# Optimization experiments

Measured on AMD Instinct MI355X. Metric: run time of the kernel, lower is better.

The kernel has to match this reference:

```python
import jax, jax.numpy as jnp
import numpy as np

NUM_CAPSULE = 16
DIM_CAPSULE = 64
ROUTINGS = 3
T_EPS = 1e-07


def squash(v, axis=-1):
    # NOTE: this repo's 'squash' is v / sqrt(||v||^2 + eps) (norm-only scaling)
    s = jnp.sum(v * v, axis=axis, keepdims=True)
    return v / jnp.sqrt(s + T_EPS)


def setup_inputs() -> dict:
    key = jax.random.key(0)
    k1, k2 = jax.random.split(key)
    B, N_in, D_in = 64, 512, 1024
    x = jax.random.normal(k1, (B, N_in, D_in), dtype=jnp.float32)
    # xavier-normal-ish init for W [1, D_in, num_capsule*dim_capsule]
    fan_in, fan_out = D_in, NUM_CAPSULE * DIM_CAPSULE
    std = float(np.sqrt(2.0 / (fan_in + fan_out)))
    W = jax.random.normal(k2, (1, D_in, NUM_CAPSULE * DIM_CAPSULE), dtype=jnp.float32) * std
    return {"x": x, "W": W}


def reference(x, W):
    B, N_in, D_in = x.shape
    # u_hat: [B, N_in, num_cap*dim_cap] -> [B, num_cap, N_in, dim_cap]
    u_hat = jnp.matmul(x, W[0])
    u_hat = u_hat.reshape(B, N_in, NUM_CAPSULE, DIM_CAPSULE).transpose(0, 2, 1, 3)
    b = jnp.zeros((B, NUM_CAPSULE, N_in), dtype=u_hat.dtype)
    outputs = None
    for i in range(ROUTINGS):
        # torch code permutes to [B, N_in, num_cap], softmaxes dim=2, permutes back:
        # equivalent to softmax over the num_capsule axis (axis=1)
        c = jax.nn.softmax(b, axis=1)  # [B, num_cap, N_in]
        outputs = squash(jnp.einsum('bij,bijk->bik', c, u_hat))  # [B, num_cap, dim_cap]
        if i < ROUTINGS - 1:
            b = jnp.einsum('bik,bijk->bij', outputs, u_hat)  # [B, num_cap, N_in]
    return outputs
```

## Files before the change

kernel.cpp:

```cpp
#include <hip/hip_runtime.h>
#include <stdint.h>

#define NUM_CAP 16
#define DIM_CAP 64
#define BATCH   64
#define N_IN    512
#define D_IN    1024
#define N_COL   1024
#define M_ROWS  (BATCH*N_IN)

typedef __attribute__((ext_vector_type(8))) short short8;
typedef __attribute__((ext_vector_type(4))) float f32x4;

__device__ __forceinline__ float bf2f(unsigned int u) {
  return __uint_as_float(u << 16);
}
__device__ __forceinline__ unsigned short f2bf_rne(float f) {
  unsigned int x = __float_as_uint(f);
  x += 0x7fffu + ((x >> 16) & 1u);
  return (unsigned short)(x >> 16);
}
__device__ __forceinline__ unsigned int pack_trunc(unsigned int lo, unsigned int hi) {
  return (lo >> 16) | (hi & 0xffff0000u);
}

__global__ void transpose_w(const float* __restrict__ W,
                            unsigned short* __restrict__ Wt) {
  __shared__ float tile[32][33];
  const int tx = threadIdx.x, ty = threadIdx.y;
  const int bx = blockIdx.x, by = blockIdx.y;
  tile[ty][tx] = W[(by * 32 + ty) * N_COL + bx * 32 + tx];
  __syncthreads();
  Wt[(bx * 32 + ty) * D_IN + by * 32 + tx] = f2bf_rne(tile[tx][ty]);
}

__global__ __launch_bounds__(256) void gemm_uhat(
    const float* __restrict__ A,
    const unsigned short* __restrict__ Bt,
    unsigned short* __restrict__ C) {
  __shared__ __align__(16) unsigned short lA[128 * 32];
  __shared__ __align__(16) unsigned short lB[128 * 32];

  const int t = threadIdx.x;
  const int wave = t >> 6, lane = t & 63;
  const int xcd = blockIdx.x & 7, local = blockIdx.x >> 3;
  const int mt = xcd * 32 + (local >> 3), nt = local & 7;
  const int m0 = mt * 128, n0 = nt * 128;
  const int wm = wave & 1, wn = wave >> 1;

  f32x4 acc[4][4] = {};

  const int ar = t >> 1, ah = t & 1;
  const float* agp = A + (size_t)(m0 + ar) * D_IN + ah * 16;
  const int xrA = (ar >> 1) & 3;
  unsigned short* lap0 = lA + ar * 32 + ((2 * ah + 0) ^ xrA) * 8;
  unsigned short* lap1 = lA + ar * 32 + ((2 * ah + 1) ^ xrA) * 8;

  const int srow = lane >> 2;
  const int schunk = ((lane & 3) ^ ((srow >> 1) & 3)) * 8;

  for (int kt = 0; kt < D_IN / 32; ++kt) {
    const int k0 = kt * 32;
    __syncthreads();
    const uint4 a0 = *(const uint4*)(agp + k0);
    const uint4 a1 = *(const uint4*)(agp + k0 + 4);
    const uint4 a2 = *(const uint4*)(agp + k0 + 8);
    const uint4 a3 = *(const uint4*)(agp + k0 + 12);
    uint4 p0, p1;
    p0.x = pack_trunc(a0.x, a0.y); p0.y = pack_trunc(a0.z, a0.w);
    p0.z = pack_trunc(a1.x, a1.y); p0.w = pack_trunc(a1.z, a1.w);
    p1.x = pack_trunc(a2.x, a2.y); p1.y = pack_trunc(a2.z, a2.w);
    p1.z = pack_trunc(a3.x, a3.y); p1.w = pack_trunc(a3.z, a3.w);
    *(uint4*)lap0 = p0;
    *(uint4*)lap1 = p1;
    #pragma unroll
    for (int s0 = 0; s0 < 2; ++s0) {
      const int s = wave + s0 * 4;
      const unsigned short* gb = Bt + (size_t)(n0 + s * 16 + srow) * D_IN + k0 + schunk;
      __builtin_amdgcn_global_load_lds(
          (const __attribute__((address_space(1))) void*)gb,
          (__attribute__((address_space(3))) void*)(lB + s * 512), 16, 0, 0);
    }
    __syncthreads();

    short8 af[4], bfr[4];
    const int rsel = lane & 15;
    const int q = lane >> 4;
    const int koff = (q ^ ((rsel >> 1) & 3)) * 8;
    #pragma unroll
    for (int tm = 0; tm < 4; tm++)
      af[tm] = *(const short8*)&lA[(wm * 64 + tm * 16 + rsel) * 32 + koff];
    #pragma unroll
    for (int tn = 0; tn < 4; tn++)
      bfr[tn] = *(const short8*)&lB[(wn * 64 + tn * 16 + rsel) * 32 + koff];
    #pragma unroll
    for (int tm = 0; tm < 4; tm++)
      #pragma unroll
      for (int tn = 0; tn < 4; tn++)
        acc[tm][tn] = __builtin_amdgcn_mfma_f32_16x16x32_bf16(
            af[tm], bfr[tn], acc[tm][tn], 0, 0, 0);
  }

  const int lrow = (lane >> 4) * 4, lcol = lane & 15;
  #pragma unroll
  for (int tm = 0; tm < 4; tm++)
    #pragma unroll
    for (int tn = 0; tn < 4; tn++)
      #pragma unroll
      for (int r = 0; r < 4; r++) {
        const int row = m0 + wm * 64 + tm * 16 + lrow + r;
        const int col = n0 + wn * 64 + tn * 16 + lcol;
        C[(size_t)row * N_COL + col] = f2bf_rne(acc[tm][tn][r]);
      }
}

__global__ __launch_bounds__(256) void route_partial(
    const unsigned short* __restrict__ uhat,
    const float* __restrict__ prev,
    float* __restrict__ P,
    const int first) {
  __shared__ float red[4][1024];
  const int t = threadIdx.x;
  const int w = t >> 6, lane = t & 63;
  const int b = blockIdx.x >> 4, jt4 = blockIdx.x & 15;
  const int jt = jt4 * 4 + w;
  const int i_l = lane >> 2, c4 = lane & 3;

  float pv[16];
  if (!first) {
    const float* pp = prev + (b * NUM_CAP + i_l) * DIM_CAP + c4 * 16;
    #pragma unroll
    for (int q = 0; q < 16; q++) pv[q] = pp[q];
  }
  float acc[16];
  #pragma unroll
  for (int q = 0; q < 16; q++) acc[q] = 0.f;

  const unsigned short* ub =
      uhat + (size_t)(b * N_IN + jt * 8) * N_COL + lane * 16;

  for (int jj = 0; jj < 8; ++jj, ub += N_COL) {
    const uint4 d0 = *(const uint4*)ub;
    const uint4 d1 = *(const uint4*)(ub + 8);
    float u[16];
    #define UNP(wd, o) { u[(o)] = bf2f((wd) & 0xffffu); u[(o)+1] = __uint_as_float((wd) & 0xffff0000u); }
    UNP(d0.x, 0) UNP(d0.y, 2) UNP(d0.z, 4) UNP(d0.w, 6)
    UNP(d1.x, 8) UNP(d1.y, 10) UNP(d1.z, 12) UNP(d1.w, 14)
    #undef UNP

    float c;
    if (first) {
      c = 0.0625f;
    } else {
      float dot = 0.f;
      #pragma unroll
      for (int q = 0; q < 16; q++) dot = fmaf(pv[q], u[q], dot);
      dot += __shfl_xor(dot, 1);
      dot += __shfl_xor(dot, 2);
      float m = dot;
      #pragma unroll
      for (int d = 4; d < 64; d <<= 1) m = fmaxf(m, __shfl_xor(m, d));
      const float e = __expf(dot - m);
      float s = e;
      #pragma unroll
      for (int d = 4; d < 64; d <<= 1) s += __shfl_xor(s, d);
      c = e / s;
    }
    #pragma unroll
    for (int q = 0; q < 16; q++) acc[q] = fmaf(c, u[q], acc[q]);
  }

  #pragma unroll
  for (int q = 0; q < 4; q++)
    *(float4*)&red[w][lane * 16 + q * 4] = make_float4(
        acc[q * 4 + 0], acc[q * 4 + 1], acc[q * 4 + 2], acc[q * 4 + 3]);
  __syncthreads();
  const float4 r0 = *(const float4*)&red[0][t * 4];
  const float4 r1 = *(const float4*)&red[1][t * 4];
  const float4 r2 = *(const float4*)&red[2][t * 4];
  const float4 r3 = *(const float4*)&red[3][t * 4];
  float4 s;
  s.x = r0.x + r1.x + r2.x + r3.x;
  s.y = r0.y + r1.y + r2.y + r3.y;
  s.z = r0.z + r1.z + r2.z + r3.z;
  s.w = r0.w + r1.w + r2.w + r3.w;
  *(float4*)&P[(size_t)blockIdx.x * 1024 + t * 4] = s;
}

__global__ __launch_bounds__(64) void route_reduce(
    const float* __restrict__ P, float* __restrict__ dst) {
  const int bi = blockIdx.x;
  const int k = threadIdx.x;
  const int b = bi >> 4, i = bi & 15;
  const float* p = P + (size_t)b * 16 * 1024 + i * 64 + k;
  float s = 0.f;
  #pragma unroll
  for (int tt = 0; tt < 16; ++tt) s += p[(size_t)tt * 1024];
  float ss = s * s;
  #pragma unroll
  for (int d = 1; d < 64; d <<= 1) ss += __shfl_xor(ss, d);
  dst[bi * 64 + k] = s / sqrtf(ss + 1e-7f);
}

extern "C" void kernel_launch(void* const* d_in, const int* in_sizes, int n_in,
                              void* d_out, int out_size, void* d_ws, size_t ws_size,
                              hipStream_t stream) {
  const float* x = (const float*)d_in[0];
  const float* W = (const float*)d_in[1];
  float* out = (float*)d_out;

  char* ws = (char*)d_ws;
  unsigned short* Wt   = (unsigned short*)ws;
  unsigned short* uhat = (unsigned short*)(ws + (size_t)(2 << 20));
  float* P    = (float*)(ws + (size_t)66 * (1 << 20));
  float* prev = (float*)(ws + (size_t)70 * (1 << 20));

  transpose_w<<<dim3(32, 32), dim3(32, 32), 0, stream>>>(W, Wt);
  gemm_uhat<<<2048, 256, 0, stream>>>(x, Wt, uhat);

  route_partial<<<1024, 256, 0, stream>>>(uhat, prev, P, 1);
  route_reduce<<<1024, 64, 0, stream>>>(P, prev);
  route_partial<<<1024, 256, 0, stream>>>(uhat, prev, P, 0);
  route_reduce<<<1024, 64, 0, stream>>>(P, prev);
  route_partial<<<1024, 256, 0, stream>>>(uhat, prev, P, 0);
  route_reduce<<<1024, 64, 0, stream>>>(P, out);
}
```

Measured before the change: 374.2 us.

## Fuse routing iterations into one per-batch kernel and prefetch A tiles in GEMM

```diff
diff --git a/kernel.cpp b/kernel.cpp
--- a/kernel.cpp
+++ b/kernel.cpp
@@ -59,13 +59,14 @@
   const int srow = lane >> 2;
   const int schunk = ((lane & 3) ^ ((srow >> 1) & 3)) * 8;
 
+  uint4 a0 = *(const uint4*)(agp);
+  uint4 a1 = *(const uint4*)(agp + 4);
+  uint4 a2 = *(const uint4*)(agp + 8);
+  uint4 a3 = *(const uint4*)(agp + 12);
+
   for (int kt = 0; kt < D_IN / 32; ++kt) {
     const int k0 = kt * 32;
     __syncthreads();
-    const uint4 a0 = *(const uint4*)(agp + k0);
-    const uint4 a1 = *(const uint4*)(agp + k0 + 4);
-    const uint4 a2 = *(const uint4*)(agp + k0 + 8);
-    const uint4 a3 = *(const uint4*)(agp + k0 + 12);
     uint4 p0, p1;
     p0.x = pack_trunc(a0.x, a0.y); p0.y = pack_trunc(a0.z, a0.w);
     p0.z = pack_trunc(a1.x, a1.y); p0.w = pack_trunc(a1.z, a1.w);
@@ -83,6 +84,12 @@
     }
     __syncthreads();
 
+    const int kn = ((kt + 1) & 31) * 32;
+    a0 = *(const uint4*)(agp + kn);
+    a1 = *(const uint4*)(agp + kn + 4);
+    a2 = *(const uint4*)(agp + kn + 8);
+    a3 = *(const uint4*)(agp + kn + 12);
+
     short8 af[4], bfr[4];
     const int rsel = lane & 15;
     const int q = lane >> 4;
@@ -114,92 +121,86 @@
       }
 }
 
-__global__ __launch_bounds__(256) void route_partial(
+__global__ __launch_bounds__(1024) void route_all(
     const unsigned short* __restrict__ uhat,
-    const float* __restrict__ prev,
-    float* __restrict__ P,
-    const int first) {
-  __shared__ float red[4][1024];
+    float* __restrict__ out) {
+  __shared__ float red[16][1028];
+  __shared__ float sq[16][68];
   const int t = threadIdx.x;
   const int w = t >> 6, lane = t & 63;
-  const int b = blockIdx.x >> 4, jt4 = blockIdx.x & 15;
-  const int jt = jt4 * 4 + w;
+  const int b = blockIdx.x;
   const int i_l = lane >> 2, c4 = lane & 3;
-
-  float pv[16];
-  if (!first) {
-    const float* pp = prev + (b * NUM_CAP + i_l) * DIM_CAP + c4 * 16;
-    #pragma unroll
-    for (int q = 0; q < 16; q++) pv[q] = pp[q];
+  const int oi = t >> 6, ok = t & 63;
+
+  const unsigned short* ub0 =
+      uhat + (size_t)(b * N_IN + w * 32) * N_COL + lane * 16;
+
+  for (int it = 0; it < 3; ++it) {
+    float pv[16];
+    if (it) {
+      #pragma unroll
+      for (int q = 0; q < 4; q++)
+        *(float4*)&pv[q * 4] = *(const float4*)&sq[i_l][c4 * 16 + q * 4];
+    }
+    float acc[16];
+    #pragma unroll
+    for (int q = 0; q < 16; q++) acc[q] = 0.f;
+
+    const unsigned short* ub = ub0;
+    for (int jj = 0; jj < 32; ++jj, ub += N_COL) {
+      const uint4 d0 = *(const uint4*)ub;
+      const uint4 d1 = *(const uint4*)(ub + 8);
+      float u[16];
+      #define UNP(wd, o) { u[(o)] = bf2f((wd) & 0xffffu); u[(o)+1] = __uint_as_float((wd) & 0xffff0000u); }
+      UNP(d0.x, 0) UNP(d0.y, 2) UNP(d0.z, 4) UNP(d0.w, 6)
+      UNP(d1.x, 8) UNP(d1.y, 10) UNP(d1.z, 12) UNP(d1.w, 14)
+      #undef UNP
+
+      float c;
+      if (it == 0) {
+        c = 0.0625f;
+      } else {
+        float dot = 0.f;
+        #pragma unroll
+        for (int q = 0; q < 16; q++) dot = fmaf(pv[q], u[q], dot);
+        dot += __shfl_xor(dot, 1);
+        dot += __shfl_xor(dot, 2);
+        float m = dot;
+        #pragma unroll
+        for (int d = 4; d < 64; d <<= 1) m = fmaxf(m, __shfl_xor(m, d));
+        const float e = __expf(dot - m);
+        float s = e;
+        #pragma unroll
+        for (int d = 4; d < 64; d <<= 1) s += __shfl_xor(s, d);
+        c = e / s;
+      }
+      #pragma unroll
+      for (int q = 0; q < 16; q++) acc[q] = fmaf(c, u[q], acc[q]);
+    }
+
+    #pragma unroll
+    for (int q = 0; q < 4; q++)
+      *(float4*)&red[w][i_l * 64 + c4 * 16 + q * 4] = make_float4(
+          acc[q * 4 + 0], acc[q * 4 + 1], acc[q * 4 + 2], acc[q * 4 + 3]);
+    __syncthreads();
+
+    float s = 0.f;
+    #pragma unroll
+    for (int ww = 0; ww < 16; ++ww) s += red[ww][t];
+
+    float ss = s * s;
+    #pragma unroll
+    for (int d = 1; d < 64; d <<= 1) ss += __shfl_xor(ss, d);
+    const float v = s / sqrtf(ss + 1e-7f);
+
+    __syncthreads();
+    if (it < 2) {
+      sq[oi][ok] = v;
+      __syncthreads();
+    } else {
+      out[b * 1024 + t] = v;
+    }
   }
-  float acc[16];
-  #pragma unroll
-  for (int q = 0; q < 16; q++) acc[q] = 0.f;
-
-  const unsigned short* ub =
-      uhat + (size_t)(b * N_IN + jt * 8) * N_COL + lane * 16;
-
-  for (int jj = 0; jj < 8; ++jj, ub += N_COL) {
-    const uint4 d0 = *(const uint4*)ub;
-    const uint4 d1 = *(const uint4*)(ub + 8);
-    float u[16];
-    #define UNP(wd, o) { u[(o)] = bf2f((wd) & 0xffffu); u[(o)+1] = __uint_as_float((wd) & 0xffff0000u); }
-    UNP(d0.x, 0) UNP(d0.y, 2) UNP(d0.z, 4) UNP(d0.w, 6)
-    UNP(d1.x, 8) UNP(d1.y, 10) UNP(d1.z, 12) UNP(d1.w, 14)
-    #undef UNP
-
-    float c;
-    if (first) {
-      c = 0.0625f;
-    } else {
-      float dot = 0.f;
-      #pragma unroll
-      for (int q = 0; q < 16; q++) dot = fmaf(pv[q], u[q], dot);
-      dot += __shfl_xor(dot, 1);
-      dot += __shfl_xor(dot, 2);
-      float m = dot;
-      #pragma unroll
-      for (int d = 4; d < 64; d <<= 1) m = fmaxf(m, __shfl_xor(m, d));
-      const float e = __expf(dot - m);
-      float s = e;
-      #pragma unroll
-      for (int d = 4; d < 64; d <<= 1) s += __shfl_xor(s, d);
-      c = e / s;
-    }
-    #pragma unroll
-    for (int q = 0; q < 16; q++) acc[q] = fmaf(c, u[q], acc[q]);
-  }
-
-  #pragma unroll
-  for (int q = 0; q < 4; q++)
-    *(float4*)&red[w][lane * 16 + q * 4] = make_float4(
-        acc[q * 4 + 0], acc[q * 4 + 1], acc[q * 4 + 2], acc[q * 4 + 3]);
-  __syncthreads();
-  const float4 r0 = *(const float4*)&red[0][t * 4];
-  const float4 r1 = *(const float4*)&red[1][t * 4];
-  const float4 r2 = *(const float4*)&red[2][t * 4];
-  const float4 r3 = *(const float4*)&red[3][t * 4];
-  float4 s;
-  s.x = r0.x + r1.x + r2.x + r3.x;
-  s.y = r0.y + r1.y + r2.y + r3.y;
-  s.z = r0.z + r1.z + r2.z + r3.z;
-  s.w = r0.w + r1.w + r2.w + r3.w;
-  *(float4*)&P[(size_t)blockIdx.x * 1024 + t * 4] = s;
-}
-
-__global__ __launch_bounds__(64) void route_reduce(
-    const float* __restrict__ P, float* __restrict__ dst) {
-  const int bi = blockIdx.x;
-  const int k = threadIdx.x;
-  const int b = bi >> 4, i = bi & 15;
-  const float* p = P + (size_t)b * 16 * 1024 + i * 64 + k;
-  float s = 0.f;
-  #pragma unroll
-  for (int tt = 0; tt < 16; ++tt) s += p[(size_t)tt * 1024];
-  float ss = s * s;
-  #pragma unroll
-  for (int d = 1; d < 64; d <<= 1) ss += __shfl_xor(ss, d);
-  dst[bi * 64 + k] = s / sqrtf(ss + 1e-7f);
 }
 
 extern "C" void kernel_launch(void* const* d_in, const int* in_sizes, int n_in,
@@ -212,16 +213,8 @@
   char* ws = (char*)d_ws;
   unsigned short* Wt   = (unsigned short*)ws;
   unsigned short* uhat = (unsigned short*)(ws + (size_t)(2 << 20));
-  float* P    = (float*)(ws + (size_t)66 * (1 << 20));
-  float* prev = (float*)(ws + (size_t)70 * (1 << 20));
 
   transpose_w<<<dim3(32, 32), dim3(32, 32), 0, stream>>>(W, Wt);
   gemm_uhat<<<2048, 256, 0, stream>>>(x, Wt, uhat);
-
-  route_partial<<<1024, 256, 0, stream>>>(uhat, prev, P, 1);
-  route_reduce<<<1024, 64, 0, stream>>>(P, prev);
-  route_partial<<<1024, 256, 0, stream>>>(uhat, prev, P, 0);
-  route_reduce<<<1024, 64, 0, stream>>>(P, prev);
-  route_partial<<<1024, 256, 0, stream>>>(uhat, prev, P, 0);
-  route_reduce<<<1024, 64, 0, stream>>>(P, out);
-}
+  route_all<<<BATCH, 1024, 0, stream>>>(uhat, out);
+}
```

Result: no change. 371.9 us (-0.6%).

## Pre-convert x to bf16, fuse first routing pass into GEMM epilogue

Applied to the files above, without the earlier changes.

```diff
diff --git a/kernel.cpp b/kernel.cpp
--- a/kernel.cpp
+++ b/kernel.cpp
@@ -20,8 +20,21 @@
   x += 0x7fffu + ((x >> 16) & 1u);
   return (unsigned short)(x >> 16);
 }
-__device__ __forceinline__ unsigned int pack_trunc(unsigned int lo, unsigned int hi) {
-  return (lo >> 16) | (hi & 0xffff0000u);
+__device__ __forceinline__ unsigned int pack_rne(unsigned int lo, unsigned int hi) {
+  const unsigned int lr = lo + (0x7fffu + ((lo >> 16) & 1u));
+  const unsigned int hr = hi + (0x7fffu + ((hi >> 16) & 1u));
+  return (lr >> 16) | (hr & 0xffff0000u);
+}
+
+__global__ __launch_bounds__(256) void conv_x(const float* __restrict__ x,
+                                              unsigned short* __restrict__ xb) {
+  const size_t i = ((size_t)blockIdx.x * 256 + threadIdx.x) * 8;
+  const uint4 a = *(const uint4*)(x + i);
+  const uint4 b = *(const uint4*)(x + i + 4);
+  uint4 p;
+  p.x = pack_rne(a.x, a.y); p.y = pack_rne(a.z, a.w);
+  p.z = pack_rne(b.x, b.y); p.w = pack_rne(b.z, b.w);
+  *(uint4*)(xb + i) = p;
 }
 
 __global__ void transpose_w(const float* __restrict__ W,
@@ -34,12 +47,19 @@
   Wt[(bx * 32 + ty) * D_IN + by * 32 + tx] = f2bf_rne(tile[tx][ty]);
 }
 
+__global__ __launch_bounds__(256) void zero_s1(float* __restrict__ S1) {
+  *(float4*)(S1 + ((size_t)blockIdx.x * 256 + threadIdx.x) * 4) =
+      make_float4(0.f, 0.f, 0.f, 0.f);
+}
+
 __global__ __launch_bounds__(256) void gemm_uhat(
-    const float* __restrict__ A,
+    const unsigned short* __restrict__ A,
     const unsigned short* __restrict__ Bt,
-    unsigned short* __restrict__ C) {
+    unsigned short* __restrict__ C,
+    float* __restrict__ S1) {
   __shared__ __align__(16) unsigned short lA[128 * 32];
   __shared__ __align__(16) unsigned short lB[128 * 32];
+  __shared__ float cs[128];
 
   const int t = threadIdx.x;
   const int wave = t >> 6, lane = t & 63;
@@ -48,13 +68,9 @@
   const int m0 = mt * 128, n0 = nt * 128;
   const int wm = wave & 1, wn = wave >> 1;
 
+  if (t < 128) cs[t] = 0.f;
+
   f32x4 acc[4][4] = {};
-
-  const int ar = t >> 1, ah = t & 1;
-  const float* agp = A + (size_t)(m0 + ar) * D_IN + ah * 16;
-  const int xrA = (ar >> 1) & 3;
-  unsigned short* lap0 = lA + ar * 32 + ((2 * ah + 0) ^ xrA) * 8;
-  unsigned short* lap1 = lA + ar * 32 + ((2 * ah + 1) ^ xrA) * 8;
 
   const int srow = lane >> 2;
   const int schunk = ((lane & 3) ^ ((srow >> 1) & 3)) * 8;
@@ -62,20 +78,13 @@
   for (int kt = 0; kt < D_IN / 32; ++kt) {
     const int k0 = kt * 32;
     __syncthreads();
-    const uint4 a0 = *(const uint4*)(agp + k0);
-    const uint4 a1 = *(const uint4*)(agp + k0 + 4);
-    const uint4 a2 = *(const uint4*)(agp + k0 + 8);
-    const uint4 a3 = *(const uint4*)(agp + k0 + 12);
-    uint4 p0, p1;
-    p0.x = pack_trunc(a0.x, a0.y); p0.y = pack_trunc(a0.z, a0.w);
-    p0.z = pack_trunc(a1.x, a1.y); p0.w = pack_trunc(a1.z, a1.w);
-    p1.x = pack_trunc(a2.x, a2.y); p1.y = pack_trunc(a2.z, a2.w);
-    p1.z = pack_trunc(a3.x, a3.y); p1.w = pack_trunc(a3.z, a3.w);
-    *(uint4*)lap0 = p0;
-    *(uint4*)lap1 = p1;
     #pragma unroll
     for (int s0 = 0; s0 < 2; ++s0) {
       const int s = wave + s0 * 4;
+      const unsigned short* ga = A + (size_t)(m0 + s * 16 + srow) * D_IN + k0 + schunk;
+      __builtin_amdgcn_global_load_lds(
+          (const __attribute__((address_space(1))) void*)ga,
+          (__attribute__((address_space(3))) void*)(lA + s * 512), 16, 0, 0);
       const unsigned short* gb = Bt + (size_t)(n0 + s * 16 + srow) * D_IN + k0 + schunk;
       __builtin_amdgcn_global_load_lds(
           (const __attribute__((address_space(1))) void*)gb,
@@ -112,13 +121,27 @@
         const int col = n0 + wn * 64 + tn * 16 + lcol;
         C[(size_t)row * N_COL + col] = f2bf_rne(acc[tm][tn][r]);
       }
-}
-
-__global__ __launch_bounds__(256) void route_partial(
+
+  #pragma unroll
+  for (int tn = 0; tn < 4; tn++) {
+    float p = 0.f;
+    #pragma unroll
+    for (int tm = 0; tm < 4; tm++)
+      #pragma unroll
+      for (int r = 0; r < 4; r++) p += acc[tm][tn][r];
+    atomicAdd(&cs[wn * 64 + tn * 16 + lcol], p);
+  }
+  __syncthreads();
+  if (t < 128)
+    atomicAdd(&S1[(size_t)(mt >> 2) * N_COL + n0 + t], cs[t] * 0.0625f);
+}
+
+__global__ __launch_bounds__(256) void route_mid(
     const unsigned short* __restrict__ uhat,
-    const float* __restrict__ prev,
-    float* __restrict__ P,
-    const int first) {
+    const float* __restrict__ Vin,
+    float* __restrict__ Pout,
+    const int mode) {
+  __shared__ float sq[16 * 68];
   __shared__ float red[4][1024];
   const int t = threadIdx.x;
   const int w = t >> 6, lane = t & 63;
@@ -126,12 +149,30 @@
   const int jt = jt4 * 4 + w;
   const int i_l = lane >> 2, c4 = lane & 3;
 
+  float4 v4;
+  if (mode == 0) {
+    v4 = *(const float4*)&Vin[(size_t)b * 1024 + t * 4];
+  } else {
+    v4 = make_float4(0.f, 0.f, 0.f, 0.f);
+    #pragma unroll
+    for (int s = 0; s < 16; ++s) {
+      const float4 ps = *(const float4*)&Vin[((size_t)b * 16 + s) * 1024 + t * 4];
+      v4.x += ps.x; v4.y += ps.y; v4.z += ps.z; v4.w += ps.w;
+    }
+  }
+  float ss = v4.x * v4.x + v4.y * v4.y + v4.z * v4.z + v4.w * v4.w;
+  #pragma unroll
+  for (int d = 1; d < 16; d <<= 1) ss += __shfl_xor(ss, d);
+  const float inv = 1.f / sqrtf(ss + 1e-7f);
+  const int oi = t >> 4, ok = (t & 15) * 4;
+  *(float4*)&sq[oi * 68 + ok] = make_float4(v4.x * inv, v4.y * inv, v4.z * inv, v4.w * inv);
+  __syncthreads();
+
   float pv[16];
-  if (!first) {
-    const float* pp = prev + (b * NUM_CAP + i_l) * DIM_CAP + c4 * 16;
-    #pragma unroll
-    for (int q = 0; q < 16; q++) pv[q] = pp[q];
-  }
+  #pragma unroll
+  for (int q = 0; q < 4; q++)
+    *(float4*)&pv[q * 4] = *(const float4*)&sq[i_l * 68 + c4 * 16 + q * 4];
+
   float acc[16];
   #pragma unroll
   for (int q = 0; q < 16; q++) acc[q] = 0.f;
@@ -148,24 +189,16 @@
     UNP(d1.x, 8) UNP(d1.y, 10) UNP(d1.z, 12) UNP(d1.w, 14)
     #undef UNP
 
-    float c;
-    if (first) {
-      c = 0.0625f;
-    } else {
-      float dot = 0.f;
-      #pragma unroll
-      for (int q = 0; q < 16; q++) dot = fmaf(pv[q], u[q], dot);
-      dot += __shfl_xor(dot, 1);
-      dot += __shfl_xor(dot, 2);
-      float m = dot;
-      #pragma unroll
-      for (int d = 4; d < 64; d <<= 1) m = fmaxf(m, __shfl_xor(m, d));
-      const float e = __expf(dot - m);
-      float s = e;
-      #pragma unroll
-      for (int d = 4; d < 64; d <<= 1) s += __shfl_xor(s, d);
-      c = e / s;
-    }
+    float dot = 0.f;
+    #pragma unroll
+    for (int q = 0; q < 16; q++) dot = fmaf(pv[q], u[q], dot);
+    dot += __shfl_xor(dot, 1);
+    dot += __shfl_xor(dot, 2);
+    const float e = __expf(dot);
+    float s = e;
+    #pragma unroll
+    for (int d = 4; d < 64; d <<= 1) s += __shfl_xor(s, d);
+    const float c = e / s;
     #pragma unroll
     for (int q = 0; q < 16; q++) acc[q] = fmaf(c, u[q], acc[q]);
   }
@@ -175,19 +208,16 @@
     *(float4*)&red[w][lane * 16 + q * 4] = make_float4(
         acc[q * 4 + 0], acc[q * 4 + 1], acc[q * 4 + 2], acc[q * 4 + 3]);
   __syncthreads();
-  const float4 r0 = *(const float4*)&red[0][t * 4];
-  const float4 r1 = *(const float4*)&red[1][t * 4];
-  const float4 r2 = *(const float4*)&red[2][t * 4];
-  const float4 r3 = *(const float4*)&red[3][t * 4];
-  float4 s;
-  s.x = r0.x + r1.x + r2.x + r3.x;
-  s.y = r0.y + r1.y + r2.y + r3.y;
-  s.z = r0.z + r1.z + r2.z + r3.z;
-  s.w = r0.w + r1.w + r2.w + r3.w;
-  *(float4*)&P[(size_t)blockIdx.x * 1024 + t * 4] = s;
-}
-
-__global__ __launch_bounds__(64) void route_reduce(
+  float4 s4 = make_float4(0.f, 0.f, 0.f, 0.f);
+  #pragma unroll
+  for (int ww = 0; ww < 4; ++ww) {
+    const float4 r = *(const float4*)&red[ww][t * 4];
+    s4.x += r.x; s4.y += r.y; s4.z += r.z; s4.w += r.w;
+  }
+  *(float4*)&Pout[(size_t)blockIdx.x * 1024 + t * 4] = s4;
+}
+
+__global__ __launch_bounds__(64) void route_last(
     const float* __restrict__ P, float* __restrict__ dst) {
   const int bi = blockIdx.x;
   const int k = threadIdx.x;
@@ -212,16 +242,17 @@
   char* ws = (char*)d_ws;
   unsigned short* Wt   = (unsigned short*)ws;
   unsigned short* uhat = (unsigned short*)(ws + (size_t)(2 << 20));
-  float* P    = (float*)(ws + (size_t)66 * (1 << 20));
-  float* prev = (float*)(ws + (size_t)70 * (1 << 20));
+  unsigned short* xb   = (unsigned short*)(ws + (size_t)66 * (1 << 20));
+  float* S1 = (float*)(ws + (size_t)130 * (1 << 20));
+  float* P1 = (float*)(ws + (size_t)66 * (1 << 20));
+  float* P2 = (float*)(ws + (size_t)71 * (1 << 20));
 
   transpose_w<<<dim3(32, 32), dim3(32, 32), 0, stream>>>(W, Wt);
-  gemm_uhat<<<2048, 256, 0, stream>>>(x, Wt, uhat);
-
-  route_partial<<<1024, 256, 0, stream>>>(uhat, prev, P, 1);
-  route_reduce<<<1024, 64, 0, stream>>>(P, prev);
-  route_partial<<<1024, 256, 0, stream>>>(uhat, prev, P, 0);
-  route_reduce<<<1024, 64, 0, stream>>>(P, prev);
-  route_partial<<<1024, 256, 0, stream>>>(uhat, prev, P, 0);
-  route_reduce<<<1024, 64, 0, stream>>>(P, out);
-}
+  conv_x<<<16384, 256, 0, stream>>>(x, xb);
+  zero_s1<<<64, 256, 0, stream>>>(S1);
+  gemm_uhat<<<2048, 256, 0, stream>>>(xb, Wt, uhat, S1);
+
+  route_mid<<<1024, 256, 0, stream>>>(uhat, S1, P1, 0);
+  route_mid<<<1024, 256, 0, stream>>>(uhat, P1, P2, 1);
+  route_last<<<1024, 64, 0, stream>>>(P2, out);
+}
```

New measurement: 339.2 us. 1.1x faster.
